# Kernel tuning notes

Measured on AMD Instinct MI355X. Metric: run time of the kernel, lower is better.

## Reference

```python
import jax, jax.numpy as jnp
import numpy as np
from jax.scipy.stats import norm

B, T = 64, 1024
RNN_DIM, EMB_DIM, ATTN_DIM = 1024, 512, 128
N_FILT, KSIZE, N_MEAN = 32, 31, 8
LOGVAR_MIN = float(np.log(0.1 ** 2))
LOGVAR_MAX = float(np.log(36.77 ** 2))


def setup_inputs() -> dict:
    key = jax.random.key(0)
    ks = jax.random.split(key, 10)
    return {
        "attention_hidden_state": jax.random.normal(ks[0], (B, RNN_DIM), jnp.float32),
        "memory": jax.random.normal(ks[1], (B, T, EMB_DIM), jnp.float32),
        "processed_memory": jax.random.normal(ks[2], (B, T, ATTN_DIM), jnp.float32),
        "attention_weights_cat": jax.random.uniform(ks[3], (B, 2, T), jnp.float32),
        "prev_means": jnp.zeros((B,), jnp.float32),
        "mask": jnp.zeros((B, T), bool),
        # learned parameters (all Linear layers bias=False; conv bias=False)
        "W_query": jax.random.normal(ks[4], (ATTN_DIM, RNN_DIM), jnp.float32) * 0.02,
        "conv_w": jax.random.normal(ks[5], (N_FILT, 2, KSIZE), jnp.float32) * 0.1,
        "W_loc": jax.random.normal(ks[6], (ATTN_DIM, N_FILT), jnp.float32) * 0.1,
        "W_mean": jax.random.normal(ks[7], (N_MEAN, ATTN_DIM), jnp.float32) * 0.05,
        "W_logvar": jax.random.normal(ks[8], (1, ATTN_DIM), jnp.float32) * 0.05,
    }


def reference(attention_hidden_state, memory, processed_memory, attention_weights_cat,
              prev_means, mask, W_query, conv_w, W_loc, W_mean, W_logvar):
    pad = (KSIZE - 1) // 2
    # query projection: [B, 1, attn_dim]
    processed_query = (attention_hidden_state @ W_query.T)[:, None, :]
    # location layer: conv1d(2 -> n_filters, same padding) then dense -> [B, T, attn_dim]
    loc = jax.lax.conv_general_dilated(
        attention_weights_cat, conv_w, window_strides=(1,),
        padding=[(pad, pad)], dimension_numbers=("NCH", "OIH", "NCH"))  # [B, F, T]
    processed_loc = jnp.einsum("bft,df->btd", loc, W_loc)
    pred = jnp.tanh(processed_query + processed_loc + processed_memory)  # [B, T, D]
    avg = pred.mean(axis=1)                                              # [B, D]
    # monotonic mean increment (soft_clip = softplus, keeps increments positive)
    mean_inc = jax.nn.softplus(avg @ W_mean.T).sum(axis=-1)              # [B]
    means = prev_means + mean_inc                                        # [B]
    logvars = (LOGVAR_MAX - LOGVAR_MIN) * jax.nn.sigmoid(avg @ W_logvar.T) + LOGVAR_MIN
    stds = jnp.exp(0.5 * logvars[:, 0])                                  # [B]
    # Gaussian window: CDF(x+0.5) - CDF(x-0.5), x = 0..T-1
    x = jnp.arange(T, dtype=jnp.float32)[None, :]                        # [1, T]
    mu, sd = means[:, None], stds[:, None]
    p = norm.cdf((x + 0.5 - mu) / sd) - norm.cdf((x - 0.5 - mu) / sd)    # [B, T]
    attention_weights = jnp.where(mask, 0.0, p)
    attention_context = jnp.einsum("bt,bte->be", attention_weights, memory)
    return attention_context, attention_weights
```

## Files before the change

kernel.cpp:

```cpp
#include <hip/hip_runtime.h>
#include <math.h>

#define B 64
#define T 1024
#define RNN_DIM 1024
#define EMB_DIM 512
#define ATTN_DIM 128
#define N_FILT 32
#define KSIZE 31
#define N_MEAN 8

#define LOGVAR_MIN (-4.605170185988091f)
#define LOGVAR_MAX (7.2093654f)

#define NX 8
#define TTILE 128
#define AWWIN 160
#define MAGIC 0x73C0FFEEu

typedef __attribute__((ext_vector_type(8))) short bf16x8;
typedef __attribute__((ext_vector_type(4))) float f32x4;

__device__ __forceinline__ unsigned short f2bf(float x) {
    unsigned u = __float_as_uint(x);
    u += 0x7FFFu + ((u >> 16) & 1u);
    return (unsigned short)(u >> 16);
}

__global__ __launch_bounds__(512, 4) void fused_kernel(
        const float* __restrict__ hidden,
        const float* __restrict__ memory,
        const float* __restrict__ pm,
        const float* __restrict__ awcat,
        const float* __restrict__ prevm,
        const unsigned char* __restrict__ mask,
        const float* __restrict__ Wq,
        const float* __restrict__ convw,
        const float* __restrict__ Wloc,
        const float* __restrict__ Wmean,
        const float* __restrict__ Wlogvar,
        unsigned* __restrict__ pqflags,
        unsigned* __restrict__ avgflags,
        float* __restrict__ pq_ws,
        float* __restrict__ avg_part,
        float* __restrict__ out_ctx,
        float* __restrict__ out_w) {
    __shared__ __align__(16) float aw_s[2][AWWIN];
    __shared__ __align__(16) float pq_s[ATTN_DIM];
    __shared__ __align__(16) unsigned short loc_bf[TTILE * 32];
    __shared__ __align__(16) unsigned short wl_bf[ATTN_DIM * 32];
    __shared__ __align__(16) float red2[8][ATTN_DIM];
    __shared__ __align__(16) float a_s[ATTN_DIM];
    __shared__ float w_s[T];
    __shared__ __align__(16) float4 cred_s[32][16];
    __shared__ float musd_s[2];
    __shared__ int slo_s[8], shi_s[8];

    const int b = blockIdx.x;
    const int x = blockIdx.y;
    const int tid = threadIdx.x;
    const int t0 = x * TTILE;
    const int lane = tid & 63;
    const int w = tid >> 6;

    for (int idx = tid; idx < 2 * AWWIN; idx += 512) {
        int c = idx / AWWIN, j = idx - c * AWWIN;
        int tg = t0 - 16 + j;
        aw_s[c][j] = (tg >= 0 && tg < T) ? awcat[(size_t)b * 2 * T + c * T + tg] : 0.f;
    }

    {
        const float4* wsrc = (const float4*)Wloc;
        float4 v0 = wsrc[tid * 2], v1 = wsrc[tid * 2 + 1];
        uint4 pk;
        pk.x = (unsigned)f2bf(v0.x) | ((unsigned)f2bf(v0.y) << 16);
        pk.y = (unsigned)f2bf(v0.z) | ((unsigned)f2bf(v0.w) << 16);
        pk.z = (unsigned)f2bf(v1.x) | ((unsigned)f2bf(v1.y) << 16);
        pk.w = (unsigned)f2bf(v1.z) | ((unsigned)f2bf(v1.w) << 16);
        *(uint4*)&wl_bf[tid * 8] = pk;
    }

    {
        const float4* h4 = (const float4*)(hidden + (size_t)b * RNN_DIM);
        float4 hv0 = h4[lane], hv1 = h4[lane + 64];
        float4 hv2 = h4[lane + 128], hv3 = h4[lane + 192];
#pragma unroll
        for (int pass = 0; pass < 2; ++pass) {
            int d = x * 16 + pass * 8 + w;
            const float4* w4 = (const float4*)(Wq + (size_t)d * RNN_DIM);
            float4 wa = w4[lane], wb = w4[lane + 64];
            float4 wc = w4[lane + 128], wd = w4[lane + 192];
            float acc = hv0.x * wa.x + hv0.y * wa.y + hv0.z * wa.z + hv0.w * wa.w;
            acc += hv1.x * wb.x + hv1.y * wb.y + hv1.z * wb.z + hv1.w * wb.w;
            acc += hv2.x * wc.x + hv2.y * wc.y + hv2.z * wc.z + hv2.w * wc.w;
            acc += hv3.x * wd.x + hv3.y * wd.y + hv3.z * wd.z + hv3.w * wd.w;
#pragma unroll
            for (int off = 32; off > 0; off >>= 1)
                acc += __shfl_xor(acc, off, 64);
            if (lane == 0)
                __hip_atomic_store(&pq_ws[b * ATTN_DIM + d], acc,
                                   __ATOMIC_RELAXED, __HIP_MEMORY_SCOPE_AGENT);
        }
        asm volatile("s_waitcnt vmcnt(0)" ::: "memory");
    }
    __syncthreads();
    if (tid == 0)
        __hip_atomic_store(&pqflags[b * NX + x], MAGIC,
                           __ATOMIC_RELEASE, __HIP_MEMORY_SCOPE_AGENT);

    {
        int f = tid & 31, o = tid >> 5;
        float s[8];
#pragma unroll
        for (int i = 0; i < 8; ++i) s[i] = 0.f;
#pragma unroll
        for (int c = 0; c < 2; ++c) {
            float cw[KSIZE];
#pragma unroll
            for (int k = 0; k < KSIZE; ++k)
                cw[k] = convw[f * 2 * KSIZE + c * KSIZE + k];
            float a[40];
#pragma unroll
            for (int j = 0; j < 10; ++j) {
                float4 v = *(const float4*)&aw_s[c][o * 8 + 4 * j];
                a[4 * j] = v.x; a[4 * j + 1] = v.y; a[4 * j + 2] = v.z; a[4 * j + 3] = v.w;
            }
#pragma unroll
            for (int i = 0; i < 8; ++i) {
                float t = 0.f;
#pragma unroll
                for (int k = 0; k < KSIZE; ++k)
                    t += a[i + k + 1] * cw[k];
                s[i] += t;
            }
        }
#pragma unroll
        for (int i = 0; i < 8; ++i)
            loc_bf[(o * 8 + i) * 32 + f] = f2bf(s[i]);
    }
    __syncthreads();

    {
        int col = lane & 15;
        int kg = lane >> 4;
        const float* pmL = pm + (size_t)(b * T + t0 + w * 16) * ATTN_DIM + col;

        float pmr[8][4];
#pragma unroll
        for (int n = 0; n < 8; ++n)
#pragma unroll
            for (int j = 0; j < 4; ++j)
                pmr[n][j] = pmL[(size_t)(kg * 4 + j) * ATTN_DIM + n * 16];

        bf16x8 bfrag[8];
#pragma unroll
        for (int n = 0; n < 8; ++n)
            bfrag[n] = *(const bf16x8*)&wl_bf[(n * 16 + col) * 32 + kg * 8];
        bf16x8 af = *(const bf16x8*)&loc_bf[(w * 16 + col) * 32 + kg * 8];

        if (tid == 0) {
#pragma unroll
            for (int s = 0; s < NX; ++s) {
                const unsigned* fp = &pqflags[b * NX + s];
                while (__hip_atomic_load(fp, __ATOMIC_RELAXED, __HIP_MEMORY_SCOPE_AGENT) != MAGIC)
                    __builtin_amdgcn_s_sleep(1);
            }
        }
        __syncthreads();
        if (tid < ATTN_DIM)
            pq_s[tid] = __hip_atomic_load(&pq_ws[b * ATTN_DIM + tid],
                                          __ATOMIC_RELAXED, __HIP_MEMORY_SCOPE_AGENT);
        __syncthreads();

        float pqv[8];
#pragma unroll
        for (int n = 0; n < 8; ++n) pqv[n] = pq_s[n * 16 + col];

        float accs[8];
#pragma unroll
        for (int n = 0; n < 8; ++n) accs[n] = 0.f;
#pragma unroll
        for (int n = 0; n < 8; ++n) {
            f32x4 c = {0.f, 0.f, 0.f, 0.f};
            c = __builtin_amdgcn_mfma_f32_16x16x32_bf16(af, bfrag[n], c, 0, 0, 0);
#pragma unroll
            for (int j = 0; j < 4; ++j) {
                float xv = c[j] + pqv[n] + pmr[n][j];
                float e = __expf(2.f * xv);
                accs[n] += 1.f - 2.f / (e + 1.f);
            }
        }
#pragma unroll
        for (int n = 0; n < 8; ++n) {
            float s = accs[n];
            s += __shfl_xor(s, 16, 64);
            s += __shfl_xor(s, 32, 64);
            if (lane < 16) red2[w][n * 16 + lane] = s;
        }
    }
    __syncthreads();

    if (tid < ATTN_DIM) {
        float s = 0.f;
#pragma unroll
        for (int w2 = 0; w2 < 8; ++w2) s += red2[w2][tid];
        __hip_atomic_store(&avg_part[((size_t)b * NX + x) * ATTN_DIM + tid], s,
                           __ATOMIC_RELAXED, __HIP_MEMORY_SCOPE_AGENT);
    }
    asm volatile("s_waitcnt vmcnt(0)" ::: "memory");
    __syncthreads();
    if (tid == 0) {
        __hip_atomic_store(&avgflags[b * NX + x], MAGIC,
                           __ATOMIC_RELEASE, __HIP_MEMORY_SCOPE_AGENT);
#pragma unroll
        for (int s = 0; s < NX; ++s) {
            const unsigned* fp = &avgflags[b * NX + s];
            while (__hip_atomic_load(fp, __ATOMIC_RELAXED, __HIP_MEMORY_SCOPE_AGENT) != MAGIC)
                __builtin_amdgcn_s_sleep(1);
        }
    }
    __syncthreads();

    if (tid < ATTN_DIM) {
        float s = 0.f;
#pragma unroll
        for (int ss = 0; ss < NX; ++ss)
            s += __hip_atomic_load(&avg_part[((size_t)b * NX + ss) * ATTN_DIM + tid],
                                   __ATOMIC_RELAXED, __HIP_MEMORY_SCOPE_AGENT);
        a_s[tid] = s * (1.f / (float)T);
    }
    __syncthreads();

    if (tid < 64) {
        float macc[N_MEAN];
#pragma unroll
        for (int m = 0; m < N_MEAN; ++m) macc[m] = 0.f;
        float lv = 0.f;
#pragma unroll
        for (int i = 0; i < 2; ++i) {
            int d = tid + i * 64;
            float a = a_s[d];
#pragma unroll
            for (int m = 0; m < N_MEAN; ++m) macc[m] += a * Wmean[m * ATTN_DIM + d];
            lv += a * Wlogvar[d];
        }
#pragma unroll
        for (int off = 32; off > 0; off >>= 1) {
#pragma unroll
            for (int m = 0; m < N_MEAN; ++m) macc[m] += __shfl_xor(macc[m], off, 64);
            lv += __shfl_xor(lv, off, 64);
        }
        if (tid == 0) {
            float mean_inc = 0.f;
#pragma unroll
            for (int m = 0; m < N_MEAN; ++m) {
                float xx = macc[m];
                mean_inc += fmaxf(xx, 0.f) + log1pf(expf(-fabsf(xx)));
            }
            float mu = prevm[b] + mean_inc;
            float sig = 1.f / (1.f + expf(-lv));
            float logvar = (LOGVAR_MAX - LOGVAR_MIN) * sig + LOGVAR_MIN;
            musd_s[0] = mu;
            musd_s[1] = 1.f / expf(0.5f * logvar);
        }
    }
    __syncthreads();

    float mu = musd_s[0];
    float rsd = musd_s[1];
    const float is2 = 0.7071067811865476f;
    int lo = T, hi = -1;
#pragma unroll
    for (int r = 0; r < 2; ++r) {
        int t = tid + r * 512;
        float z1 = ((float)t + 0.5f - mu) * rsd * is2;
        float z2 = ((float)t - 0.5f - mu) * rsd * is2;
        float p = 0.5f * (erff(z1) - erff(z2));
        if (mask[(size_t)b * T + t]) p = 0.f;
        w_s[t] = p;
        if ((t >> 7) == x) out_w[(size_t)b * T + t] = p;
        if (p != 0.f) { lo = min(lo, t); hi = max(hi, t); }
    }
#pragma unroll
    for (int off = 32; off > 0; off >>= 1) {
        lo = min(lo, __shfl_xor(lo, off, 64));
        hi = max(hi, __shfl_xor(hi, off, 64));
    }
    if (lane == 0) { slo_s[w] = lo; shi_s[w] = hi; }
    __syncthreads();
#pragma unroll
    for (int wv = 0; wv < 8; ++wv) {
        lo = min(lo, slo_s[wv]);
        hi = max(hi, shi_s[wv]);
    }

    {
        int e = tid & 15;
        int e4 = x * 16 + e;
        int trow = tid >> 4;
        const float4* m4 = (const float4*)memory + (size_t)b * T * (EMB_DIM / 4);
        float4 acc = make_float4(0.f, 0.f, 0.f, 0.f);
        for (int t = lo + trow; t <= hi; t += 32) {
            float wvv = w_s[t];
            float4 mm = m4[(size_t)t * (EMB_DIM / 4) + e4];
            acc.x += wvv * mm.x;
            acc.y += wvv * mm.y;
            acc.z += wvv * mm.z;
            acc.w += wvv * mm.w;
        }
        cred_s[trow][e] = acc;
        __syncthreads();
#pragma unroll
        for (int step = 16; step >= 1; step >>= 1) {
            if (trow < step) {
                float4 o = cred_s[trow + step][e];
                cred_s[trow][e].x += o.x;
                cred_s[trow][e].y += o.y;
                cred_s[trow][e].z += o.z;
                cred_s[trow][e].w += o.w;
            }
            __syncthreads();
        }
        if (tid < 16)
            ((float4*)(out_ctx + (size_t)b * EMB_DIM))[e4] = cred_s[0][e];
    }
}

extern "C" void kernel_launch(void* const* d_in, const int* in_sizes, int n_in,
                              void* d_out, int out_size, void* d_ws, size_t ws_size,
                              hipStream_t stream) {
    const float* hidden  = (const float*)d_in[0];
    const float* memory  = (const float*)d_in[1];
    const float* pm      = (const float*)d_in[2];
    const float* awcat   = (const float*)d_in[3];
    const float* prevm   = (const float*)d_in[4];
    const unsigned char* mask = (const unsigned char*)d_in[5];
    const float* Wq      = (const float*)d_in[6];
    const float* convw   = (const float*)d_in[7];
    const float* Wloc    = (const float*)d_in[8];
    const float* Wmean   = (const float*)d_in[9];
    const float* Wlogvar = (const float*)d_in[10];

    unsigned* pqflags  = (unsigned*)d_ws;
    unsigned* avgflags = pqflags + B * NX;
    float* pq_ws       = (float*)d_ws + 1024;
    float* avg_part    = pq_ws + B * ATTN_DIM;

    float* out_ctx = (float*)d_out;
    float* out_w   = out_ctx + B * EMB_DIM;

    fused_kernel<<<dim3(B, NX), 512, 0, stream>>>(
        hidden, memory, pm, awcat, prevm, mask, Wq, convw, Wloc, Wmean,
        Wlogvar, pqflags, avgflags, pq_ws, avg_part, out_ctx, out_w);
}
```

Baseline: 34.35 us.

## Split attention-dim across blocks and exchange conv output via global workspace

Each block of a batch row now owns a 16-wide slice of the attention dimension across all T positions, rather than a 128-position time tile across all 128 dims. The conv output is written to global memory as bf16 and shared between blocks through per-tile flags. This removes the cross-block exchange of the query projection and the 8-way partial-average summation. In exchange it adds a global round-trip for the location features plus spin-waits on flags from other blocks. processed_memory reads become strided 16-float slices instead of full rows.

```diff
diff --git a/kernel.cpp b/kernel.cpp
--- a/kernel.cpp
+++ b/kernel.cpp
@@ -14,7 +14,8 @@
 #define LOGVAR_MAX (7.2093654f)
 
 #define NX 8
-#define TTILE 128
+#define DSL 16
+#define TSL 128
 #define AWWIN 160
 #define MAGIC 0x73C0FFEEu
 
@@ -39,17 +40,16 @@
         const float* __restrict__ Wloc,
         const float* __restrict__ Wmean,
         const float* __restrict__ Wlogvar,
-        unsigned* __restrict__ pqflags,
+        unsigned* __restrict__ locflags,
         unsigned* __restrict__ avgflags,
-        float* __restrict__ pq_ws,
-        float* __restrict__ avg_part,
+        unsigned short* __restrict__ loc_ws,
+        float* __restrict__ avg_ws,
         float* __restrict__ out_ctx,
         float* __restrict__ out_w) {
     __shared__ __align__(16) float aw_s[2][AWWIN];
-    __shared__ __align__(16) float pq_s[ATTN_DIM];
-    __shared__ __align__(16) unsigned short loc_bf[TTILE * 32];
-    __shared__ __align__(16) unsigned short wl_bf[ATTN_DIM * 32];
-    __shared__ __align__(16) float red2[8][ATTN_DIM];
+    __shared__ __align__(16) unsigned short wl_bf[DSL * 32];
+    __shared__ __align__(16) float pq_s[DSL];
+    __shared__ __align__(16) float red2[8][DSL];
     __shared__ __align__(16) float a_s[ATTN_DIM];
     __shared__ float w_s[T];
     __shared__ __align__(16) float4 cred_s[32][16];
@@ -59,9 +59,10 @@
     const int b = blockIdx.x;
     const int x = blockIdx.y;
     const int tid = threadIdx.x;
-    const int t0 = x * TTILE;
     const int lane = tid & 63;
     const int w = tid >> 6;
+    const int t0 = x * TSL;
+    const int dlo = x * DSL;
 
     for (int idx = tid; idx < 2 * AWWIN; idx += 512) {
         int c = idx / AWWIN, j = idx - c * AWWIN;
@@ -69,16 +70,54 @@
         aw_s[c][j] = (tg >= 0 && tg < T) ? awcat[(size_t)b * 2 * T + c * T + tg] : 0.f;
     }
 
-    {
-        const float4* wsrc = (const float4*)Wloc;
-        float4 v0 = wsrc[tid * 2], v1 = wsrc[tid * 2 + 1];
+    if (tid < 64) {
+        int i = tid >> 2, seg = tid & 3;
+        const float4* wsrc = (const float4*)(Wloc + (size_t)(dlo + i) * 32) + seg * 2;
+        float4 v0 = wsrc[0], v1 = wsrc[1];
         uint4 pk;
         pk.x = (unsigned)f2bf(v0.x) | ((unsigned)f2bf(v0.y) << 16);
         pk.y = (unsigned)f2bf(v0.z) | ((unsigned)f2bf(v0.w) << 16);
         pk.z = (unsigned)f2bf(v1.x) | ((unsigned)f2bf(v1.y) << 16);
         pk.w = (unsigned)f2bf(v1.z) | ((unsigned)f2bf(v1.w) << 16);
-        *(uint4*)&wl_bf[tid * 8] = pk;
-    }
+        *(uint4*)&wl_bf[i * 32 + seg * 8] = pk;
+    }
+    __syncthreads();
+
+    {
+        int f = tid & 31, o = tid >> 5;
+        float s[8];
+#pragma unroll
+        for (int i = 0; i < 8; ++i) s[i] = 0.f;
+#pragma unroll
+        for (int c = 0; c < 2; ++c) {
+            float cw[KSIZE];
+#pragma unroll
+            for (int k = 0; k < KSIZE; ++k)
+                cw[k] = convw[f * 2 * KSIZE + c * KSIZE + k];
+            float a[40];
+#pragma unroll
+            for (int j = 0; j < 10; ++j) {
+                float4 v = *(const float4*)&aw_s[c][o * 8 + 4 * j];
+                a[4 * j] = v.x; a[4 * j + 1] = v.y; a[4 * j + 2] = v.z; a[4 * j + 3] = v.w;
+            }
+#pragma unroll
+            for (int i = 0; i < 8; ++i) {
+                float t = 0.f;
+#pragma unroll
+                for (int k = 0; k < KSIZE; ++k)
+                    t += a[i + k + 1] * cw[k];
+                s[i] += t;
+            }
+        }
+#pragma unroll
+        for (int i = 0; i < 8; ++i)
+            loc_ws[((size_t)b * T + t0 + o * 8 + i) * 32 + f] = f2bf(s[i]);
+    }
+    asm volatile("s_waitcnt vmcnt(0)" ::: "memory");
+    __syncthreads();
+    if (tid == 0)
+        __hip_atomic_store(&locflags[b * NX + x], MAGIC,
+                           __ATOMIC_RELEASE, __HIP_MEMORY_SCOPE_AGENT);
 
     {
         const float4* h4 = (const float4*)(hidden + (size_t)b * RNN_DIM);
@@ -86,8 +125,8 @@
         float4 hv2 = h4[lane + 128], hv3 = h4[lane + 192];
 #pragma unroll
         for (int pass = 0; pass < 2; ++pass) {
-            int d = x * 16 + pass * 8 + w;
-            const float4* w4 = (const float4*)(Wq + (size_t)d * RNN_DIM);
+            int dl = pass * 8 + w;
+            const float4* w4 = (const float4*)(Wq + (size_t)(dlo + dl) * RNN_DIM);
             float4 wa = w4[lane], wb = w4[lane + 64];
             float4 wc = w4[lane + 128], wd = w4[lane + 192];
             float acc = hv0.x * wa.x + hv0.y * wa.y + hv0.z * wa.z + hv0.w * wa.w;
@@ -97,114 +136,57 @@
 #pragma unroll
             for (int off = 32; off > 0; off >>= 1)
                 acc += __shfl_xor(acc, off, 64);
-            if (lane == 0)
-                __hip_atomic_store(&pq_ws[b * ATTN_DIM + d], acc,
-                                   __ATOMIC_RELAXED, __HIP_MEMORY_SCOPE_AGENT);
-        }
-        asm volatile("s_waitcnt vmcnt(0)" ::: "memory");
-    }
-    __syncthreads();
-    if (tid == 0)
-        __hip_atomic_store(&pqflags[b * NX + x], MAGIC,
-                           __ATOMIC_RELEASE, __HIP_MEMORY_SCOPE_AGENT);
-
-    {
-        int f = tid & 31, o = tid >> 5;
-        float s[8];
-#pragma unroll
-        for (int i = 0; i < 8; ++i) s[i] = 0.f;
-#pragma unroll
-        for (int c = 0; c < 2; ++c) {
-            float cw[KSIZE];
-#pragma unroll
-            for (int k = 0; k < KSIZE; ++k)
-                cw[k] = convw[f * 2 * KSIZE + c * KSIZE + k];
-            float a[40];
-#pragma unroll
-            for (int j = 0; j < 10; ++j) {
-                float4 v = *(const float4*)&aw_s[c][o * 8 + 4 * j];
-                a[4 * j] = v.x; a[4 * j + 1] = v.y; a[4 * j + 2] = v.z; a[4 * j + 3] = v.w;
-            }
-#pragma unroll
-            for (int i = 0; i < 8; ++i) {
-                float t = 0.f;
-#pragma unroll
-                for (int k = 0; k < KSIZE; ++k)
-                    t += a[i + k + 1] * cw[k];
-                s[i] += t;
-            }
-        }
-#pragma unroll
-        for (int i = 0; i < 8; ++i)
-            loc_bf[(o * 8 + i) * 32 + f] = f2bf(s[i]);
+            if (lane == 0) pq_s[dl] = acc;
+        }
     }
     __syncthreads();
 
     {
         int col = lane & 15;
         int kg = lane >> 4;
-        const float* pmL = pm + (size_t)(b * T + t0 + w * 16) * ATTN_DIM + col;
-
+        const unsigned* fp = &locflags[b * NX + w];
+        while (__hip_atomic_load(fp, __ATOMIC_RELAXED, __HIP_MEMORY_SCOPE_AGENT) != MAGIC)
+            __builtin_amdgcn_s_sleep(1);
+
+        bf16x8 bfrag = *(const bf16x8*)&wl_bf[col * 32 + kg * 8];
+        float pqv = pq_s[col];
+        const unsigned short* locL = loc_ws + ((size_t)b * T + w * TSL) * 32;
+        const float* pmB = pm + ((size_t)b * T + w * TSL) * ATTN_DIM;
+
+        bf16x8 af[8];
+#pragma unroll
+        for (int m = 0; m < 8; ++m)
+            af[m] = *(const bf16x8*)&locL[(m * 16 + col) * 32 + kg * 8];
         float pmr[8][4];
 #pragma unroll
-        for (int n = 0; n < 8; ++n)
+        for (int m = 0; m < 8; ++m)
 #pragma unroll
             for (int j = 0; j < 4; ++j)
-                pmr[n][j] = pmL[(size_t)(kg * 4 + j) * ATTN_DIM + n * 16];
-
-        bf16x8 bfrag[8];
-#pragma unroll
-        for (int n = 0; n < 8; ++n)
-            bfrag[n] = *(const bf16x8*)&wl_bf[(n * 16 + col) * 32 + kg * 8];
-        bf16x8 af = *(const bf16x8*)&loc_bf[(w * 16 + col) * 32 + kg * 8];
-
-        if (tid == 0) {
-#pragma unroll
-            for (int s = 0; s < NX; ++s) {
-                const unsigned* fp = &pqflags[b * NX + s];
-                while (__hip_atomic_load(fp, __ATOMIC_RELAXED, __HIP_MEMORY_SCOPE_AGENT) != MAGIC)
-                    __builtin_amdgcn_s_sleep(1);
-            }
-        }
-        __syncthreads();
-        if (tid < ATTN_DIM)
-            pq_s[tid] = __hip_atomic_load(&pq_ws[b * ATTN_DIM + tid],
-                                          __ATOMIC_RELAXED, __HIP_MEMORY_SCOPE_AGENT);
-        __syncthreads();
-
-        float pqv[8];
-#pragma unroll
-        for (int n = 0; n < 8; ++n) pqv[n] = pq_s[n * 16 + col];
-
-        float accs[8];
-#pragma unroll
-        for (int n = 0; n < 8; ++n) accs[n] = 0.f;
-#pragma unroll
-        for (int n = 0; n < 8; ++n) {
+                pmr[m][j] = pmB[(size_t)(m * 16 + kg * 4 + j) * ATTN_DIM + dlo + col];
+
+        float acc = 0.f;
+#pragma unroll
+        for (int m = 0; m < 8; ++m) {
             f32x4 c = {0.f, 0.f, 0.f, 0.f};
-            c = __builtin_amdgcn_mfma_f32_16x16x32_bf16(af, bfrag[n], c, 0, 0, 0);
+            c = __builtin_amdgcn_mfma_f32_16x16x32_bf16(af[m], bfrag, c, 0, 0, 0);
 #pragma unroll
             for (int j = 0; j < 4; ++j) {
-                float xv = c[j] + pqv[n] + pmr[n][j];
+                float xv = c[j] + pqv + pmr[m][j];
                 float e = __expf(2.f * xv);
-                accs[n] += 1.f - 2.f / (e + 1.f);
-            }
-        }
-#pragma unroll
-        for (int n = 0; n < 8; ++n) {
-            float s = accs[n];
-            s += __shfl_xor(s, 16, 64);
-            s += __shfl_xor(s, 32, 64);
-            if (lane < 16) red2[w][n * 16 + lane] = s;
-        }
-    }
-    __syncthreads();
-
-    if (tid < ATTN_DIM) {
+                acc += 1.f - 2.f / (e + 1.f);
+            }
+        }
+        acc += __shfl_xor(acc, 16, 64);
+        acc += __shfl_xor(acc, 32, 64);
+        if (lane < 16) red2[w][lane] = acc;
+    }
+    __syncthreads();
+
+    if (tid < DSL) {
         float s = 0.f;
 #pragma unroll
         for (int w2 = 0; w2 < 8; ++w2) s += red2[w2][tid];
-        __hip_atomic_store(&avg_part[((size_t)b * NX + x) * ATTN_DIM + tid], s,
+        __hip_atomic_store(&avg_ws[b * ATTN_DIM + dlo + tid], s * (1.f / (float)T),
                            __ATOMIC_RELAXED, __HIP_MEMORY_SCOPE_AGENT);
     }
     asm volatile("s_waitcnt vmcnt(0)" ::: "memory");
@@ -220,15 +202,9 @@
         }
     }
     __syncthreads();
-
-    if (tid < ATTN_DIM) {
-        float s = 0.f;
-#pragma unroll
-        for (int ss = 0; ss < NX; ++ss)
-            s += __hip_atomic_load(&avg_part[((size_t)b * NX + ss) * ATTN_DIM + tid],
-                                   __ATOMIC_RELAXED, __HIP_MEMORY_SCOPE_AGENT);
-        a_s[tid] = s * (1.f / (float)T);
-    }
+    if (tid < ATTN_DIM)
+        a_s[tid] = __hip_atomic_load(&avg_ws[b * ATTN_DIM + tid],
+                                     __ATOMIC_RELAXED, __HIP_MEMORY_SCOPE_AGENT);
     __syncthreads();
 
     if (tid < 64) {
@@ -341,15 +317,16 @@
     const float* Wmean   = (const float*)d_in[9];
     const float* Wlogvar = (const float*)d_in[10];
 
-    unsigned* pqflags  = (unsigned*)d_ws;
-    unsigned* avgflags = pqflags + B * NX;
-    float* pq_ws       = (float*)d_ws + 1024;
-    float* avg_part    = pq_ws + B * ATTN_DIM;
+    char* ws = (char*)d_ws;
+    unsigned* locflags       = (unsigned*)ws;
+    unsigned* avgflags       = (unsigned*)(ws + 2048);
+    float* avg_ws            = (float*)(ws + 4096);
+    unsigned short* loc_ws   = (unsigned short*)(ws + 4096 + 32768);
 
     float* out_ctx = (float*)d_out;
     float* out_w   = out_ctx + B * EMB_DIM;
 
     fused_kernel<<<dim3(B, NX), 512, 0, stream>>>(
         hidden, memory, pm, awcat, prevm, mask, Wq, convw, Wloc, Wmean,
-        Wlogvar, pqflags, avgflags, pq_ws, avg_part, out_ctx, out_w);
+        Wlogvar, locflags, avgflags, loc_ws, avg_ws, out_ctx, out_w);
 }
```

Result: slower. 42.69 us (+24.3%).
